# Optimization experiments

Measured on AMD Instinct MI355X. Metric: run time of the kernel, lower is better.

Reference implementation:

```python
import jax, jax.numpy as jnp
import numpy as np

IN_F, OUT_F, TOKENS = 4096, 11008, 4096


def setup_inputs() -> dict:
    key = jax.random.key(0)
    k1, k2, k3, k4, k5 = jax.random.split(key, 5)
    x = jax.random.normal(k1, (TOKENS, IN_F), dtype=jnp.float32)
    # uint8-range quantized weights stored as int32 (harness dtype constraint)
    weight_quant = jax.random.randint(k2, (OUT_F, IN_F), 0, 255, dtype=jnp.int32)
    # per-output-channel scale (small positive) and zero-point near mid-range
    scale = jax.random.uniform(k3, (OUT_F,), dtype=jnp.float32) * 0.02 + 0.001
    zero = jax.random.uniform(k4, (OUT_F,), dtype=jnp.float32) * 255.0
    bias = jax.random.normal(k5, (OUT_F,), dtype=jnp.float32)
    return {"x": x, "weight_quant": weight_quant, "scale": scale, "zero": zero, "bias": bias}


def reference(x, weight_quant, scale, zero, bias):
    # dequantize per output channel: W = (W_q - zero) * scale, shape [out, in]
    W = (weight_quant.astype(jnp.float32) - zero[:, None]) * scale[:, None]
    # y = x @ W^T + bias -> [tokens, out]
    return jnp.einsum('ti,oi->to', x, W) + bias
```

## Files before the change

### kernel.cpp

```cpp
#include <hip/hip_runtime.h>

typedef unsigned short u16;
typedef unsigned int   u32;
typedef unsigned long long u64;
typedef signed char    i8;

typedef int   i32x4 __attribute__((ext_vector_type(4)));

#define IN_F   4096
#define OUT_F  11008
#define TOKENS 4096

#define BM 256
#define BN 128
#define BKQ 64
#define MT (TOKENS / BM)
#define NT (OUT_F / BN)
#define KT64 (IN_F / BKQ)

#define GLOAD_LDS16(g, l)                                                        \
    __builtin_amdgcn_global_load_lds(                                            \
        (const __attribute__((address_space(1))) u32*)(u64)(g),                  \
        (__attribute__((address_space(3))) u32*)(u64)(l), 16, 0, 0)

#define BAR() __builtin_amdgcn_s_barrier()
#define VM(N) asm volatile("s_waitcnt vmcnt(" #N ")" ::: "memory")

__device__ __forceinline__ int pack4(int a, int b, int c, int d) {
    return (a & 255) | ((b & 255) << 8) | ((c & 255) << 16) | (d << 24);
}

__global__ __launch_bounds__(256) void prep_x_kernel(
    const float* __restrict__ x, i8* __restrict__ xq,
    float* __restrict__ rowsum, float* __restrict__ rowscale) {
    const int row = blockIdx.x;
    const int tid = threadIdx.x;
    const float4* xr = reinterpret_cast<const float4*>(x + (size_t)row * IN_F);
    float4 v[4];
    float s = 0.f, mx = 0.f;
#pragma unroll
    for (int i = 0; i < 4; ++i) {
        v[i] = xr[tid * 4 + i];
        s += v[i].x + v[i].y + v[i].z + v[i].w;
        mx = fmaxf(mx, fmaxf(fmaxf(fabsf(v[i].x), fabsf(v[i].y)),
                             fmaxf(fabsf(v[i].z), fabsf(v[i].w))));
    }
#pragma unroll
    for (int off = 32; off > 0; off >>= 1) {
        s += __shfl_down(s, off, 64);
        mx = fmaxf(mx, __shfl_down(mx, off, 64));
    }
    __shared__ float ss[4], sm[4];
    if ((tid & 63) == 0) { ss[tid >> 6] = s; sm[tid >> 6] = mx; }
    __syncthreads();
    const float tot = ss[0] + ss[1] + ss[2] + ss[3];
    const float m4  = fmaxf(fmaxf(sm[0], sm[1]), fmaxf(sm[2], sm[3]));
    const float mg  = fmaxf(m4, 1e-20f);
    const float inv = 127.0f / mg;
    if (tid == 0) { rowsum[row] = tot; rowscale[row] = mg * (1.0f / 127.0f); }
    int4 o;
    int q[16];
#pragma unroll
    for (int i = 0; i < 4; ++i) {
        q[4 * i + 0] = (int)rintf(v[i].x * inv);
        q[4 * i + 1] = (int)rintf(v[i].y * inv);
        q[4 * i + 2] = (int)rintf(v[i].z * inv);
        q[4 * i + 3] = (int)rintf(v[i].w * inv);
    }
    o.x = pack4(q[0], q[1], q[2], q[3]);
    o.y = pack4(q[4], q[5], q[6], q[7]);
    o.z = pack4(q[8], q[9], q[10], q[11]);
    o.w = pack4(q[12], q[13], q[14], q[15]);
    reinterpret_cast<int4*>(xq + (size_t)row * IN_F)[tid] = o;
}

__global__ __launch_bounds__(256) void prep_w_kernel(
    const int* __restrict__ wq, i8* __restrict__ wb) {
    const size_t total16 = (size_t)OUT_F * IN_F / 16;
    size_t i = (size_t)blockIdx.x * blockDim.x + threadIdx.x;
    const size_t stride = (size_t)gridDim.x * blockDim.x;
    const int4* p = reinterpret_cast<const int4*>(wq);
    int4* o = reinterpret_cast<int4*>(wb);
    for (; i < total16; i += stride) {
        int4 a = p[i * 4], b = p[i * 4 + 1], c = p[i * 4 + 2], d = p[i * 4 + 3];
        int4 v;
        v.x = pack4(a.x - 128, a.y - 128, a.z - 128, a.w - 128);
        v.y = pack4(b.x - 128, b.y - 128, b.z - 128, b.w - 128);
        v.z = pack4(c.x - 128, c.y - 128, c.z - 128, c.w - 128);
        v.w = pack4(d.x - 128, d.y - 128, d.z - 128, d.w - 128);
        o[i] = v;
    }
}


#define LDA(S)                                                                    \
    _Pragma("unroll") for (int m = 0; m < 8; ++m)                                 \
        af[m] = *(const i32x4*)((const char*)&AS[S][0] +                          \
            ((wr * 128 + m * 16 + l15) * 64 + ((kq ^ ((l15 >> 1) & 3)) << 4)));

#define LDB(S, NH)                                                                \
    _Pragma("unroll") for (int n = 0; n < 2; ++n)                                 \
        bfr[n] = *(const i32x4*)((const char*)&BS[S][0] +                         \
            ((wc * 64 + ((NH) * 2 + n) * 16 + l15) * 64 +                         \
             ((kq ^ ((l15 >> 1) & 3)) << 4)));

#define MFMA_H(NH)                                                                \
    __builtin_amdgcn_s_setprio(1);                                                \
    _Pragma("unroll") for (int m = 0; m < 8; ++m)                                 \
    _Pragma("unroll") for (int n = 0; n < 2; ++n)                                 \
        acc[m][(NH) * 2 + n] = __builtin_amdgcn_mfma_i32_16x16x64_i8(             \
            af[m], bfr[n], acc[m][(NH) * 2 + n], 0, 0, 0);                        \
    __builtin_amdgcn_s_setprio(0);

#define STAGE_A(S, KT)                                                            \
    _Pragma("unroll") for (int j = 0; j < 4; ++j) {                               \
        const i8* g_ = Abase + (size_t)(w * 64 + j * 16 + (lane >> 2)) * IN_F +   \
                       (KT) * BKQ + sa16;                                         \
        GLOAD_LDS16(g_, (char*)&AS[S][0] + (w * 4 + j) * 1024);                   \
    }

#define STAGE_B(S, KT)                                                            \
    _Pragma("unroll") for (int j = 0; j < 2; ++j) {                               \
        const i8* g_ = Bbase + (size_t)(w * 32 + j * 16 + (lane >> 2)) * IN_F +   \
                       (KT) * BKQ + sa16;                                         \
        GLOAD_LDS16(g_, (char*)&BS[S][0] + (w * 2 + j) * 1024);                   \
    }

#define PHASE(S, SN, T)                                                           \
    STAGE_A(SN, (T) + 2);                                                         \
    STAGE_B(SN, (T) + 2);                                                         \
    LDA(S);                                                                       \
    LDB(S, 0);                                                                    \
    BAR();                                                                        \
    MFMA_H(0);                                                                    \
    LDB(S, 1);                                                                    \
    MFMA_H(1);                                                                    \
    VM(6);                                                                        \
    BAR();

__global__ __launch_bounds__(256, 2) void qgemm_kernel(
    const i8* __restrict__ Xq, const i8* __restrict__ Wqb,
    const float* __restrict__ rowsum, const float* __restrict__ rowscale,
    const float* __restrict__ scale, const float* __restrict__ zero,
    const float* __restrict__ bias, float* __restrict__ out) {
    __shared__ i8 AS[3][BM * BKQ];
    __shared__ i8 BS[3][BN * BKQ];

    const int bid = blockIdx.x;
    const int xcd = bid & 7;
    const int g   = bid >> 3;
    const int mt  = (xcd >> 1) * 4 + (g & 3);
    const int nt  = (xcd & 1) * 43 + (g >> 2);

    const int tid  = threadIdx.x;
    const int w    = tid >> 6;
    const int lane = tid & 63;
    const int wr   = w >> 1;
    const int wc   = w & 1;
    const int l15  = lane & 15;
    const int kq   = lane >> 4;
    const int sa16 = (((lane & 3) ^ ((lane >> 3) & 3)) << 4);

    const i8* Abase = Xq  + (size_t)mt * BM * IN_F;
    const i8* Bbase = Wqb + (size_t)nt * BN * IN_F;

    i32x4 af[8];
    i32x4 bfr[2];
    i32x4 acc[8][4];
    const i32x4 zi = {0, 0, 0, 0};
#pragma unroll
    for (int m = 0; m < 8; ++m)
#pragma unroll
        for (int n = 0; n < 4; ++n) acc[m][n] = zi;

    STAGE_A(0, 0);
    STAGE_B(0, 0);
    STAGE_A(1, 1);
    STAGE_B(1, 1);
    VM(6);
    BAR();

    for (int i = 0; i < 20; ++i) {
        const int t = 3 * i;
        PHASE(0, 2, t);
        PHASE(1, 0, t + 1);
        PHASE(2, 1, t + 2);
    }
    PHASE(0, 2, 60);
    PHASE(1, 0, 61);
    LDA(2);
    LDB(2, 0);
    BAR();
    MFMA_H(0);
    LDB(2, 1);
    MFMA_H(1);
    VM(0);
    BAR();
    LDA(0);
    LDB(0, 0);
    BAR();
    MFMA_H(0);
    LDB(0, 1);
    MFMA_H(1);

    const int rowt = mt * BM + wr * 128;
    const int colt = nt * BN + wc * 64;

    float scn[4], bcn[4], ccn[4];
#pragma unroll
    for (int n = 0; n < 4; ++n) {
        const int col = colt + n * 16 + l15;
        scn[n] = scale[col];
        bcn[n] = scn[n] * (128.0f - zero[col]);
        ccn[n] = bias[col];
    }
#pragma unroll
    for (int m = 0; m < 8; ++m) {
#pragma unroll
        for (int j = 0; j < 4; ++j) {
            const int r = rowt + m * 16 + kq * 4 + j;
            const float rsv = rowsum[r];
            const float sxv = rowscale[r];
#pragma unroll
            for (int n = 0; n < 4; ++n) {
                out[(size_t)r * OUT_F + colt + n * 16 + l15] =
                    scn[n] * (sxv * (float)acc[m][n][j]) + bcn[n] * rsv + ccn[n];
            }
        }
    }
}

extern "C" void kernel_launch(void* const* d_in, const int* in_sizes, int n_in,
                              void* d_out, int out_size, void* d_ws, size_t ws_size,
                              hipStream_t stream) {
    const float* x     = (const float*)d_in[0];
    const int*   wq    = (const int*)d_in[1];
    const float* scale = (const float*)d_in[2];
    const float* zero  = (const float*)d_in[3];
    const float* bias  = (const float*)d_in[4];
    float* out = (float*)d_out;

    char* ws = (char*)d_ws;
    i8* Wqb = (i8*)ws;
    i8* Xq  = (i8*)(ws + (size_t)OUT_F * IN_F);
    float* rowsum   = (float*)(ws + (size_t)OUT_F * IN_F + (size_t)TOKENS * IN_F);
    float* rowscale = rowsum + TOKENS;

    prep_w_kernel<<<2048, 256, 0, stream>>>(wq, Wqb);
    prep_x_kernel<<<TOKENS, 256, 0, stream>>>(x, Xq, rowsum, rowscale);
    qgemm_kernel<<<MT * NT, 256, 0, stream>>>(Xq, Wqb, rowsum, rowscale,
                                              scale, zero, bias, out);
}
```

Baseline: 257.1 us.

## Enlarge int8 GEMM tile to 256x256x128 with 8 waves and double buffering

The quantized GEMM block tile grows from 256x128 to 256x256, the K step from 64 to 128 bytes, and the block from 256 to 512 threads (one block per CU). LDS staging drops from three buffers to two, with a wider XOR swizzle for the 128-byte rows, and the XCD-to-tile mapping is rewritten for the new grid. The aim is more operand reuse per loaded byte and fewer barriers per unit of MFMA work. In exchange, each phase now waits for all outstanding loads (vmcnt 0), so load/compute overlap is shallower, and occupancy drops to a single 8-wave block per CU.

```diff
diff --git a/kernel.cpp b/kernel.cpp
--- a/kernel.cpp
+++ b/kernel.cpp
@@ -12,11 +12,11 @@
 #define TOKENS 4096
 
 #define BM 256
-#define BN 128
-#define BKQ 64
+#define BN 256
+#define BKQ 128
 #define MT (TOKENS / BM)
 #define NT (OUT_F / BN)
-#define KT64 (IN_F / BKQ)
+#define KTILES (IN_F / BKQ)
 
 #define GLOAD_LDS16(g, l)                                                        \
     __builtin_amdgcn_global_load_lds(                                            \
@@ -93,79 +93,86 @@
 }
 
 
-#define LDA(S)                                                                    \
-    _Pragma("unroll") for (int m = 0; m < 8; ++m)                                 \
-        af[m] = *(const i32x4*)((const char*)&AS[S][0] +                          \
-            ((wr * 128 + m * 16 + l15) * 64 + ((kq ^ ((l15 >> 1) & 3)) << 4)));
-
-#define LDB(S, NH)                                                                \
-    _Pragma("unroll") for (int n = 0; n < 2; ++n)                                 \
-        bfr[n] = *(const i32x4*)((const char*)&BS[S][0] +                         \
-            ((wc * 64 + ((NH) * 2 + n) * 16 + l15) * 64 +                         \
-             ((kq ^ ((l15 >> 1) & 3)) << 4)));
-
-#define MFMA_H(NH)                                                                \
+#define LDA2(S)                                                                   \
+    _Pragma("unroll") for (int m = 0; m < 8; ++m) {                               \
+        const char* rb_ = (const char*)&AS[S][0] +                                \
+                          (wr * 128 + m * 16 + l15) * 128;                        \
+        af0[m] = *(const i32x4*)(rb_ + (((kq) ^ l7) << 4));                       \
+        af1[m] = *(const i32x4*)(rb_ + (((4 + kq) ^ l7) << 4));                   \
+    }
+
+#define LDB2(S)                                                                   \
+    _Pragma("unroll") for (int n = 0; n < 4; ++n) {                               \
+        const char* rb_ = (const char*)&BS[S][0] +                                \
+                          (wc * 64 + n * 16 + l15) * 128;                         \
+        bfr0[n] = *(const i32x4*)(rb_ + (((kq) ^ l7) << 4));                      \
+        bfr1[n] = *(const i32x4*)(rb_ + (((4 + kq) ^ l7) << 4));                  \
+    }
+
+#define MFMA_KH(AF, BF)                                                           \
     __builtin_amdgcn_s_setprio(1);                                                \
     _Pragma("unroll") for (int m = 0; m < 8; ++m)                                 \
-    _Pragma("unroll") for (int n = 0; n < 2; ++n)                                 \
-        acc[m][(NH) * 2 + n] = __builtin_amdgcn_mfma_i32_16x16x64_i8(             \
-            af[m], bfr[n], acc[m][(NH) * 2 + n], 0, 0, 0);                        \
+    _Pragma("unroll") for (int n = 0; n < 4; ++n)                                 \
+        acc[m][n] = __builtin_amdgcn_mfma_i32_16x16x64_i8(                        \
+            AF[m], BF[n], acc[m][n], 0, 0, 0);                                    \
     __builtin_amdgcn_s_setprio(0);
 
 #define STAGE_A(S, KT)                                                            \
     _Pragma("unroll") for (int j = 0; j < 4; ++j) {                               \
-        const i8* g_ = Abase + (size_t)(w * 64 + j * 16 + (lane >> 2)) * IN_F +   \
-                       (KT) * BKQ + sa16;                                         \
-        GLOAD_LDS16(g_, (char*)&AS[S][0] + (w * 4 + j) * 1024);                   \
+        const int c_ = w * 4 + j;                                                 \
+        const i8* g_ = Abase + (size_t)(c_ * 8 + (lane >> 3)) * IN_F +            \
+                       (KT) * BKQ + sa;                                           \
+        GLOAD_LDS16(g_, (char*)&AS[S][0] + c_ * 1024);                            \
     }
 
 #define STAGE_B(S, KT)                                                            \
-    _Pragma("unroll") for (int j = 0; j < 2; ++j) {                               \
-        const i8* g_ = Bbase + (size_t)(w * 32 + j * 16 + (lane >> 2)) * IN_F +   \
-                       (KT) * BKQ + sa16;                                         \
-        GLOAD_LDS16(g_, (char*)&BS[S][0] + (w * 2 + j) * 1024);                   \
-    }
-
-#define PHASE(S, SN, T)                                                           \
-    STAGE_A(SN, (T) + 2);                                                         \
-    STAGE_B(SN, (T) + 2);                                                         \
-    LDA(S);                                                                       \
-    LDB(S, 0);                                                                    \
+    _Pragma("unroll") for (int j = 0; j < 4; ++j) {                               \
+        const int c_ = w * 4 + j;                                                 \
+        const i8* g_ = Bbase + (size_t)(c_ * 8 + (lane >> 3)) * IN_F +            \
+                       (KT) * BKQ + sa;                                           \
+        GLOAD_LDS16(g_, (char*)&BS[S][0] + c_ * 1024);                            \
+    }
+
+#define PHASE(S, T)                                                               \
+    STAGE_A((S) ^ 1, (T) + 1);                                                    \
+    STAGE_B((S) ^ 1, (T) + 1);                                                    \
+    LDA2(S);                                                                      \
+    LDB2(S);                                                                      \
     BAR();                                                                        \
-    MFMA_H(0);                                                                    \
-    LDB(S, 1);                                                                    \
-    MFMA_H(1);                                                                    \
-    VM(6);                                                                        \
+    MFMA_KH(af0, bfr0);                                                           \
+    MFMA_KH(af1, bfr1);                                                           \
+    VM(0);                                                                        \
     BAR();
 
-__global__ __launch_bounds__(256, 2) void qgemm_kernel(
+__global__ __launch_bounds__(512, 1) void qgemm_kernel(
     const i8* __restrict__ Xq, const i8* __restrict__ Wqb,
     const float* __restrict__ rowsum, const float* __restrict__ rowscale,
     const float* __restrict__ scale, const float* __restrict__ zero,
     const float* __restrict__ bias, float* __restrict__ out) {
-    __shared__ i8 AS[3][BM * BKQ];
-    __shared__ i8 BS[3][BN * BKQ];
+    __shared__ i8 AS[2][BM * BKQ];
+    __shared__ i8 BS[2][BN * BKQ];
 
     const int bid = blockIdx.x;
     const int xcd = bid & 7;
     const int g   = bid >> 3;
-    const int mt  = (xcd >> 1) * 4 + (g & 3);
-    const int nt  = (xcd & 1) * 43 + (g >> 2);
+    const int mt  = xcd * 2 + (g & 1);
+    const int nt  = g >> 1;
 
     const int tid  = threadIdx.x;
     const int w    = tid >> 6;
     const int lane = tid & 63;
-    const int wr   = w >> 1;
-    const int wc   = w & 1;
+    const int wr   = w >> 2;
+    const int wc   = w & 3;
     const int l15  = lane & 15;
+    const int l7   = l15 & 7;
     const int kq   = lane >> 4;
-    const int sa16 = (((lane & 3) ^ ((lane >> 3) & 3)) << 4);
+    const int sa = (((lane & 7) ^ ((lane >> 3) & 7)) << 4);
 
     const i8* Abase = Xq  + (size_t)mt * BM * IN_F;
     const i8* Bbase = Wqb + (size_t)nt * BN * IN_F;
 
-    i32x4 af[8];
-    i32x4 bfr[2];
+    i32x4 af0[8], af1[8];
+    i32x4 bfr0[4], bfr1[4];
     i32x4 acc[8][4];
     const i32x4 zi = {0, 0, 0, 0};
 #pragma unroll
@@ -175,33 +182,21 @@
 
     STAGE_A(0, 0);
     STAGE_B(0, 0);
-    STAGE_A(1, 1);
-    STAGE_B(1, 1);
-    VM(6);
-    BAR();
-
-    for (int i = 0; i < 20; ++i) {
-        const int t = 3 * i;
-        PHASE(0, 2, t);
-        PHASE(1, 0, t + 1);
-        PHASE(2, 1, t + 2);
-    }
-    PHASE(0, 2, 60);
-    PHASE(1, 0, 61);
-    LDA(2);
-    LDB(2, 0);
-    BAR();
-    MFMA_H(0);
-    LDB(2, 1);
-    MFMA_H(1);
     VM(0);
     BAR();
-    LDA(0);
-    LDB(0, 0);
+
+    PHASE(0, 0);
+#pragma unroll 1
+    for (int i = 0; i < 15; ++i) {
+        const int t = 2 * i + 1;
+        PHASE(1, t);
+        PHASE(0, t + 1);
+    }
+    LDA2(1);
+    LDB2(1);
     BAR();
-    MFMA_H(0);
-    LDB(0, 1);
-    MFMA_H(1);
+    MFMA_KH(af0, bfr0);
+    MFMA_KH(af1, bfr1);
 
     const int rowt = mt * BM + wr * 128;
     const int colt = nt * BN + wc * 64;
@@ -248,6 +243,6 @@
 
     prep_w_kernel<<<2048, 256, 0, stream>>>(wq, Wqb);
     prep_x_kernel<<<TOKENS, 256, 0, stream>>>(x, Xq, rowsum, rowscale);
-    qgemm_kernel<<<MT * NT, 256, 0, stream>>>(Xq, Wqb, rowsum, rowscale,
+    qgemm_kernel<<<MT * NT, 512, 0, stream>>>(Xq, Wqb, rowsum, rowscale,
                                               scale, zero, bias, out);
 }
```

Measured after the change: 359.5 us. +39.8%, slower.
